# Kernel tuning notes

Measured on AMD Instinct MI355X. Metric: run time of the kernel, lower is better.

## Reference

```python
import jax, jax.numpy as jnp
import numpy as np

C_A = 768; C_S = 384; C_Z = 128; H = 16; D = C_A // H
B = 1; N = 4096; NQ = 32; NK = 128; NB = N // NQ
EPS = 1e-5


def _ln(x):
    # layernorm without learned affine (affine applied by caller where present)
    m = jnp.mean(x, axis=-1, keepdims=True)
    v = jnp.mean((x - m) ** 2, axis=-1, keepdims=True)
    return (x - m) * jax.lax.rsqrt(v + EPS)


def setup_inputs() -> dict:
    key = jax.random.key(0)
    ks = jax.random.split(key, 16)
    w = lambda k, shp: jax.random.normal(k, shp, dtype=jnp.float32) * 0.02
    return dict(
        a=jax.random.normal(ks[0], (B, N, C_A), jnp.float32),
        s=jax.random.normal(ks[1], (B, N, C_S), jnp.float32),
        z=jax.random.normal(ks[2], (B, NB, NQ, NK, C_Z), jnp.float32),
        adaln_gamma_s=jnp.ones((C_S,), jnp.float32),
        adaln_ws=w(ks[3], (C_S, C_A)),
        adaln_bs=jnp.zeros((C_A,), jnp.float32),
        adaln_wskip=w(ks[4], (C_S, C_A)),
        lnz_gamma=jnp.ones((C_Z,), jnp.float32),
        wz=w(ks[5], (C_Z, H)),
        wq=w(ks[6], (C_A, C_A)), bq=jnp.zeros((C_A,), jnp.float32),
        wk=w(ks[7], (C_A, C_A)),
        wv=w(ks[8], (C_A, C_A)),
        wg=w(ks[9], (C_A, C_A)), bg=jnp.ones((C_A,), jnp.float32),
        wo=w(ks[10], (C_A, C_A)), bo=jnp.zeros((C_A,), jnp.float32),
        w_last=w(ks[11], (C_S, C_A)),
        b_last=jnp.full((C_A,), -2.0, jnp.float32),  # biasinit = -2.0
        n_queries=NQ, n_keys=NK,
    )


def _forward(a, s, z, adaln_gamma_s, adaln_ws, adaln_bs, adaln_wskip,
             lnz_gamma, wz, wq, bq, wk, wv, wg, bg, wo, bo,
             w_last, b_last, n_queries, n_keys):
    Bq, Nq, _ = a.shape
    nb = Nq // n_queries
    # AdaptiveLayerNorm (AF3 Alg 26): a <- sigmoid(Lin(s_ln)) * LN(a) + LinNoBias(s_ln)
    s_ln = _ln(s) * adaln_gamma_s
    a_ln = jax.nn.sigmoid(s_ln @ adaln_ws + adaln_bs) * _ln(a) + s_ln @ adaln_wskip
    # pair bias: LN(z) (no offset) -> per-head bias, permuted to [B,H,nb,nq,nk]
    bias = (_ln(z) * lnz_gamma) @ wz                    # [B, nb, nq, nk, H]
    bias = jnp.transpose(bias, (0, 4, 1, 2, 3))          # [B, H, nb, nq, nk]
    # projections (q has bias; k/v no bias)
    q = (a_ln @ wq + bq).reshape(Bq, nb, n_queries, H, D)
    k = (a_ln @ wk).reshape(Bq, Nq, H, D)
    v = (a_ln @ wv).reshape(Bq, Nq, H, D)
    # local window: query block w covers [w*nq, (w+1)*nq); keys are nk centered on it
    start = jnp.arange(nb) * n_queries + n_queries // 2 - n_keys // 2
    kidx = start[:, None] + jnp.arange(n_keys)[None, :]  # [nb, nk]
    valid = (kidx >= 0) & (kidx < Nq)
    kidx = jnp.clip(kidx, 0, Nq - 1)
    k_loc = k[:, kidx]                                    # [B, nb, nk, H, D]
    v_loc = v[:, kidx]
    scale = 1.0 / float(np.sqrt(D))
    scores = jnp.einsum('bwqhd,bwkhd->bhwqk', q, k_loc) * scale + bias
    scores = jnp.where(valid[None, None, :, None, :], scores, -1e9)
    p = jax.nn.softmax(scores, axis=-1)
    o = jnp.einsum('bhwqk,bwkhd->bwqhd', p, v_loc).reshape(Bq, Nq, C_A)
    # gating, output projection, final sigmoid gate from raw s
    o = (jax.nn.sigmoid(a_ln @ wg + bg) * o) @ wo + bo
    return jax.nn.sigmoid(s @ w_last + b_last) * o


def reference(a, s, z, adaln_gamma_s, adaln_ws, adaln_bs, adaln_wskip,
              lnz_gamma, wz, wq, bq, wk, wv, wg, bg, wo, bo,
              w_last, b_last, n_queries, n_keys):
    return _forward(a, s, z, adaln_gamma_s, adaln_ws, adaln_bs, adaln_wskip,
                    lnz_gamma, wz, wq, bq, wk, wv, wg, bg, wo, bo,
                    w_last, b_last, n_queries, n_keys)
```

## Files before the change

kernel.cpp:

```cpp
#include <hip/hip_runtime.h>
#include <hip/hip_bf16.h>
#include <math.h>

#define N_TOK 4096
#define CA 768
#define CS 384
#define CZ 128
#define NHEAD 16
#define DH 48
#define NQW 32
#define NKW 128
#define NBLK 128

typedef __attribute__((ext_vector_type(8))) short short8;
typedef __attribute__((ext_vector_type(4))) float float4v;
typedef __attribute__((ext_vector_type(4))) unsigned short ushort4v;

__device__ __forceinline__ float sigmoidf_(float x){ return 1.0f/(1.0f+__expf(-x)); }

__device__ __forceinline__ unsigned short f2bf(float x){
  unsigned u = __float_as_uint(x);
  unsigned r = (u + 0x7FFFu + ((u>>16)&1u)) >> 16;
  return (unsigned short)r;
}
__device__ __forceinline__ float bf2f(unsigned short b){
  return __uint_as_float(((unsigned)b)<<16);
}
__device__ __forceinline__ short8 cvt8(const float* xv){
  union { short8 v; unsigned short u[8]; } H;
  #pragma unroll
  for (int j=0;j<8;j++) H.u[j] = f2bf(xv[j]);
  return H.v;
}
__device__ __forceinline__ short8 cvt8pk(const float* x){
  union { short8 v; unsigned u32[4]; } H;
  #pragma unroll
  for (int i=0;i<4;i++)
    asm("v_cvt_pk_bf16_f32 %0, %1, %2" : "=v"(H.u32[i]) : "v"(x[2*i]), "v"(x[2*i+1]));
  return H.v;
}

__device__ __forceinline__ void gload_lds16(const void* gsrc, void* ldst){
  __builtin_amdgcn_global_load_lds(
    (const __attribute__((address_space(1))) void*)gsrc,
    (__attribute__((address_space(3))) void*)ldst, 16, 0, 0);
}

__device__ __forceinline__ int xcd_swz(int wg, int nwg){
  int cpx = nwg >> 3;
  return (wg & 7)*cpx + (wg >> 3);
}

__global__ __launch_bounds__(256) void prep_zbias_kernel(
  const float* __restrict__ z, const float* __restrict__ lnz_gamma,
  const float* __restrict__ wz, unsigned short* __restrict__ bias3,
  const float* __restrict__ s, const float* __restrict__ adaln_gamma,
  unsigned short* __restrict__ s_ln_h, unsigned short* __restrict__ s_h,
  const float* __restrict__ a, float* __restrict__ a_n,
  const float* __restrict__ ws, const float* __restrict__ wskip,
  const float* __restrict__ wq, const float* __restrict__ wk,
  const float* __restrict__ wv, const float* __restrict__ wg,
  const float* __restrict__ wo, const float* __restrict__ wlast,
  unsigned short* __restrict__ Wt1, unsigned short* __restrict__ Wt2,
  unsigned short* __restrict__ Wt3, unsigned short* __restrict__ Wt4,
  const float* __restrict__ bq, const float* __restrict__ bg,
  float* __restrict__ biasq)
{
  union PZ {
    float tile[64][65];
    float zbuf[2][2][2048];
  };
  __shared__ PZ sm;
  int bid = blockIdx.x;
  int tid = threadIdx.x;

  if (bid < 2048){
    int wave = tid>>6, lane = tid&63;
    if (wave >= 2) return;
    int lr = lane&15, quad = lane>>4;

    short8 bwh[4];
    float w1 = 0.f;
    #pragma unroll
    for (int ks=0;ks<4;ks++){
      float wv_[8];
      #pragma unroll
      for (int j=0;j<8;j++){
        int k = ks*32 + quad*8 + j;
        wv_[j] = wz[k*NHEAD + lr]*lnz_gamma[k];
        w1 += wv_[j];
      }
      bwh[ks] = cvt8pk(wv_);
    }
    w1 += __shfl_xor(w1, 16);
    w1 += __shfl_xor(w1, 32);

    size_t group = (size_t)bid*2 + wave;
    const float* zg = z + group*(size_t)(NKW*CZ);
    unsigned short* outg = bias3 + group*2048;

    int rsub = lane>>5;
    int csw  = lane&31;
    auto stage = [&](int buf, int b){
      #pragma unroll
      for (int i=0;i<8;i++){
        int r  = 2*i + rsub;
        int gc = csw ^ (r & 7);
        gload_lds16(zg + (size_t)(b*16 + r)*CZ + gc*4, &sm.zbuf[wave][buf][i*256]);
      }
    };

    stage(0, 0);
    int buf = 0;
    #pragma unroll 1
    for (int b=0; b<8; ++b){
      if (b < 7){
        stage(buf^1, b+1);
        asm volatile("s_waitcnt vmcnt(8)" ::: "memory");
      } else {
        asm volatile("s_waitcnt vmcnt(0)" ::: "memory");
      }
      __builtin_amdgcn_sched_barrier(0);

      const float* rowp = &sm.zbuf[wave][buf][lr*128];
      int sswz = lr & 7;
      float4 p[8];
      #pragma unroll
      for (int ks=0;ks<4;ks++){
        int c0 = ks*8 + quad*2;
        p[ks*2]   = *(const float4*)(rowp + (size_t)((c0  )^sswz)*4);
        p[ks*2+1] = *(const float4*)(rowp + (size_t)((c0+1)^sswz)*4);
      }
      float sum=0.f, sq=0.f;
      #pragma unroll
      for (int t=0;t<8;t++){
        sum += p[t].x + p[t].y + p[t].z + p[t].w;
        sq  += p[t].x*p[t].x + p[t].y*p[t].y + p[t].z*p[t].z + p[t].w*p[t].w;
      }
      sum += __shfl_xor(sum,16); sum += __shfl_xor(sum,32);
      sq  += __shfl_xor(sq,16);  sq  += __shfl_xor(sq,32);
      float mean = sum*(1.f/CZ);
      float var  = sq*(1.f/CZ) - mean*mean;
      float rs = rsqrtf(var + 1e-5f);

      float4v c = (float4v){0.f,0.f,0.f,0.f};
      #pragma unroll
      for (int ks=0;ks<4;ks++){
        float xv[8];
        xv[0]=p[ks*2].x;   xv[1]=p[ks*2].y;   xv[2]=p[ks*2].z;   xv[3]=p[ks*2].w;
        xv[4]=p[ks*2+1].x; xv[5]=p[ks*2+1].y; xv[6]=p[ks*2+1].z; xv[7]=p[ks*2+1].w;
        c = __builtin_amdgcn_mfma_f32_16x16x32_bf16(cvt8pk(xv), bwh[ks], c, 0,0,0);
      }

      ushort4v o4;
      #pragma unroll
      for (int r=0;r<4;r++){
        int rrow = quad*4 + r;
        float m_r  = __shfl(mean, rrow);
        float rs_r = __shfl(rs, rrow);
        o4[r] = f2bf(rs_r*(c[r] - m_r*w1));
      }
      *(ushort4v*)(outg + lr*128 + b*16 + quad*4) = o4;
      buf ^= 1;
    }
    return;
  }
  bid -= 2048;

  if (bid < 1024){
    int wave = tid>>6, lane = tid&63;
    int row = bid*4 + wave;
    const float* x = s + (size_t)row*CS;
    float v[6]; float sum=0.f, sq=0.f;
    #pragma unroll
    for (int i=0;i<6;i++){ v[i]=x[lane+64*i]; sum+=v[i]; sq+=v[i]*v[i]; }
    #pragma unroll
    for (int off=32; off; off>>=1){ sum+=__shfl_xor(sum,off); sq+=__shfl_xor(sq,off); }
    float m = sum*(1.f/CS);
    float var = sq*(1.f/CS)-m*m;
    float rs = rsqrtf(var+1e-5f);
    #pragma unroll
    for (int i=0;i<6;i++){
      int c = lane+64*i;
      s_ln_h[(size_t)row*CS+c] = f2bf((v[i]-m)*rs*adaln_gamma[c]);
      s_h[(size_t)row*CS+c]    = f2bf(v[i]);
    }
    return;
  }
  bid -= 1024;

  if (bid < 1024){
    int wave = tid>>6, lane = tid&63;
    int row = bid*4 + wave;
    const float* x = a + (size_t)row*CA;
    float v[12]; float sum=0.f, sq=0.f;
    #pragma unroll
    for (int i=0;i<12;i++){ v[i]=x[lane+64*i]; sum+=v[i]; sq+=v[i]*v[i]; }
    #pragma unroll
    for (int off=32; off; off>>=1){ sum+=__shfl_xor(sum,off); sq+=__shfl_xor(sq,off); }
    float m = sum*(1.f/CA);
    float var = sq*(1.f/CA)-m*m;
    float rs = rsqrtf(var+1e-5f);
    float* o = a_n + (size_t)row*CA;
    #pragma unroll
    for (int i=0;i<12;i++) o[lane+64*i] = (v[i]-m)*rs;
    return;
  }
  bid -= 1024;

  if (bid < 936){
    const float* src; unsigned short* dst; int K; int local;
    if      (bid < 72)  { src=ws;    dst=Wt1;                   K=CS; local=bid; }
    else if (bid < 144) { src=wskip; dst=Wt1 + (size_t)768*CS;  K=CS; local=bid-72; }
    else if (bid < 288) { src=wq;    dst=Wt2;                   K=CA; local=bid-144; }
    else if (bid < 432) { src=wk;    dst=Wt2 + (size_t)768*CA;  K=CA; local=bid-288; }
    else if (bid < 576) { src=wv;    dst=Wt2 + (size_t)1536*CA; K=CA; local=bid-432; }
    else if (bid < 720) { src=wg;    dst=Wt2 + (size_t)2304*CA; K=CA; local=bid-576; }
    else if (bid < 864) { src=wo;    dst=Wt3;                   K=CA; local=bid-720; }
    else                { src=wlast; dst=Wt4;                   K=CS; local=bid-864; }
    int ktiles = K/64;
    int kb = (local % ktiles)*64, nb = (local / ktiles)*64;
    int c = tid & 63, r0 = tid >> 6;
    #pragma unroll
    for (int i=0;i<16;i++){
      int r = r0 + 4*i;
      sm.tile[r][c] = src[(size_t)(kb+r)*CA + nb + c];
    }
    __syncthreads();
    #pragma unroll
    for (int i=0;i<16;i++){
      int r = r0 + 4*i;
      dst[(size_t)(nb+r)*K + kb + c] = f2bf(sm.tile[c][r]);
    }
    return;
  }
  bid -= 936;

  int i = bid*256 + tid;
  float v = 0.f;
  if (i < 768) v = bq[i];
  else if (i >= 2304) v = bg[i-2304];
  biasq[i] = v;
}

__global__ __launch_bounds__(256) void adaln_gemm(
  const unsigned short* __restrict__ A, const unsigned short* __restrict__ Bt,
  const float* __restrict__ bs, const float* __restrict__ a_n,
  unsigned short* __restrict__ outh)
{
  __shared__ unsigned short Ash[64*32];
  __shared__ unsigned short B1sh[128*32];
  __shared__ unsigned short B2sh[128*32];

  int tid = threadIdx.x;
  int w = tid >> 6, lane = tid & 63;
  int lr = lane & 15, quad = lane >> 4;
  int wg = xcd_swz(blockIdx.y*gridDim.x + blockIdx.x, gridDim.x*gridDim.y);
  int bx = wg % gridDim.x, by = wg / gridDim.x;
  int m0 = by*64, n0 = bx*128;
  int mbase = (w&1)*32, nbase = (w>>1)*64;

  float4v acc1[2][4], acc2[2][4];
  #pragma unroll
  for (int i=0;i<2;i++)
    #pragma unroll
    for (int j=0;j<4;j++){
      acc1[i][j] = (float4v){0.f,0.f,0.f,0.f};
      acc2[i][j] = (float4v){0.f,0.f,0.f,0.f};
    }

  int growB = w*32 + (lane>>2);
  int growA = w*16 + (lane>>2);
  int gcol8 = (lane&3)*8;

  for (int k0=0; k0<CS; k0+=32){
    __syncthreads();
    gload_lds16(A + (size_t)(m0 + growA)*CS + k0 + gcol8, &Ash[(w*16)*32]);
    #pragma unroll
    for (int i=0;i<2;i++){
      int rB = growB + i*16;
      gload_lds16(Bt + (size_t)(n0 + rB)*CS + k0 + gcol8, &B1sh[(w*32 + i*16)*32]);
      gload_lds16(Bt + (size_t)(768 + n0 + rB)*CS + k0 + gcol8, &B2sh[(w*32 + i*16)*32]);
    }
    __syncthreads();

    short8 af[2], b1f[4], b2f[4];
    #pragma unroll
    for (int mi=0;mi<2;mi++)
      af[mi] = *(const short8*)&Ash[(mbase + mi*16 + lr)*32 + quad*8];
    #pragma unroll
    for (int ni=0;ni<4;ni++){
      b1f[ni] = *(const short8*)&B1sh[(nbase + ni*16 + lr)*32 + quad*8];
      b2f[ni] = *(const short8*)&B2sh[(nbase + ni*16 + lr)*32 + quad*8];
    }
    #pragma unroll
    for (int mi=0;mi<2;mi++)
      #pragma unroll
      for (int ni=0;ni<4;ni++){
        acc1[mi][ni] = __builtin_amdgcn_mfma_f32_16x16x32_bf16(af[mi], b1f[ni], acc1[mi][ni], 0,0,0);
        acc2[mi][ni] = __builtin_amdgcn_mfma_f32_16x16x32_bf16(af[mi], b2f[ni], acc2[mi][ni], 0,0,0);
      }
  }

  #pragma unroll
  for (int ni=0;ni<4;ni++){
    int col = n0 + nbase + ni*16 + lr;
    float bsv = bs[col];
    #pragma unroll
    for (int mi=0;mi<2;mi++){
      #pragma unroll
      for (int reg=0;reg<4;reg++){
        int row = m0 + mbase + mi*16 + quad*4 + reg;
        float v = sigmoidf_(acc1[mi][ni][reg] + bsv)*a_n[(size_t)row*CA + col] + acc2[mi][ni][reg];
        outh[(size_t)row*CA + col] = f2bf(v);
      }
    }
  }
}

__global__ __launch_bounds__(256) void final_gemm(
  const unsigned short* __restrict__ A1, const unsigned short* __restrict__ B1,
  const float* __restrict__ bias1,
  const unsigned short* __restrict__ A2, const unsigned short* __restrict__ B2,
  const float* __restrict__ bias2,
  float* __restrict__ outp)
{
  __shared__ unsigned short Ash[64*32];
  __shared__ unsigned short Bsh[128*32];

  int tid = threadIdx.x;
  int w = tid >> 6, lane = tid & 63;
  int lr = lane & 15, quad = lane >> 4;
  int wg = xcd_swz(blockIdx.y*gridDim.x + blockIdx.x, gridDim.x*gridDim.y);
  int bx = wg % gridDim.x, by = wg / gridDim.x;
  int m0 = by*64, n0 = bx*128;
  int mbase = (w&1)*32, nbase = (w>>1)*64;

  float4v acc1[2][4], acc2[2][4];
  #pragma unroll
  for (int i=0;i<2;i++)
    #pragma unroll
    for (int j=0;j<4;j++){
      acc1[i][j] = (float4v){0.f,0.f,0.f,0.f};
      acc2[i][j] = (float4v){0.f,0.f,0.f,0.f};
    }

  int growB = w*32 + (lane>>2);
  int growA = w*16 + (lane>>2);
  int gcol8 = (lane&3)*8;

  const int NT1 = CA/32, NT2 = CS/32, NT = NT1+NT2;
  #pragma unroll 1
  for (int t=0; t<NT; ++t){
    const unsigned short* Ap; const unsigned short* Bp; int K, k0;
    if (t < NT1){ Ap=A1; Bp=B1; K=CA; k0=t*32; }
    else        { Ap=A2; Bp=B2; K=CS; k0=(t-NT1)*32; }
    __syncthreads();
    gload_lds16(Ap + (size_t)(m0 + growA)*K + k0 + gcol8, &Ash[(w*16)*32]);
    #pragma unroll
    for (int i=0;i<2;i++){
      int rB = growB + i*16;
      gload_lds16(Bp + (size_t)(n0 + rB)*K + k0 + gcol8, &Bsh[(w*32 + i*16)*32]);
    }
    __syncthreads();

    short8 af[2], bf[4];
    #pragma unroll
    for (int mi=0;mi<2;mi++)
      af[mi] = *(const short8*)&Ash[(mbase + mi*16 + lr)*32 + quad*8];
    #pragma unroll
    for (int ni=0;ni<4;ni++)
      bf[ni] = *(const short8*)&Bsh[(nbase + ni*16 + lr)*32 + quad*8];
    if (t < NT1){
      #pragma unroll
      for (int mi=0;mi<2;mi++)
        #pragma unroll
        for (int ni=0;ni<4;ni++)
          acc1[mi][ni] = __builtin_amdgcn_mfma_f32_16x16x32_bf16(af[mi], bf[ni], acc1[mi][ni], 0,0,0);
    } else {
      #pragma unroll
      for (int mi=0;mi<2;mi++)
        #pragma unroll
        for (int ni=0;ni<4;ni++)
          acc2[mi][ni] = __builtin_amdgcn_mfma_f32_16x16x32_bf16(af[mi], bf[ni], acc2[mi][ni], 0,0,0);
    }
  }

  #pragma unroll
  for (int ni=0;ni<4;ni++){
    int col = n0 + nbase + ni*16 + lr;
    float bv1 = bias1[col];
    float bv2 = bias2[col];
    #pragma unroll
    for (int mi=0;mi<2;mi++){
      #pragma unroll
      for (int reg=0;reg<4;reg++){
        int row = m0 + mbase + mi*16 + quad*4 + reg;
        outp[(size_t)row*CA + col] = sigmoidf_(acc2[mi][ni][reg] + bv2)*(acc1[mi][ni][reg] + bv1);
      }
    }
  }
}

__global__ __launch_bounds__(256) void qkvg_gemm(
  const unsigned short* __restrict__ A1, const unsigned short* __restrict__ B1,
  const float* __restrict__ bias1, unsigned short* __restrict__ outp)
{
  __shared__ unsigned short Ash[128*32];
  __shared__ unsigned short Bsh[128*32];

  int tid = threadIdx.x;
  int w = tid >> 6, lane = tid & 63;
  int lr = lane & 15, quad = lane >> 4;
  int wg = xcd_swz(blockIdx.y*gridDim.x + blockIdx.x, gridDim.x*gridDim.y);
  int bx = wg % gridDim.x, by = wg / gridDim.x;
  int m0 = by*128, n0 = bx*128;
  int mbase = (w&1)*64, nbase = (w>>1)*64;

  float4v acc1[4][4];
  #pragma unroll
  for (int i=0;i<4;i++)
    #pragma unroll
    for (int j=0;j<4;j++)
      acc1[i][j] = (float4v){0.f,0.f,0.f,0.f};

  int grow = w*32 + (lane>>2);
  int gcol8 = (lane&3)*8;

  for (int k0=0; k0<CA; k0+=32){
    __syncthreads();
    #pragma unroll
    for (int i=0;i<2;i++){
      int rA = grow + i*16;
      gload_lds16(A1 + (size_t)(m0 + rA)*CA + k0 + gcol8, &Ash[(w*32 + i*16)*32]);
      gload_lds16(B1 + (size_t)(n0 + rA)*CA + k0 + gcol8, &Bsh[(w*32 + i*16)*32]);
    }
    __syncthreads();

    short8 af[4], bf[4];
    #pragma unroll
    for (int mi=0;mi<4;mi++)
      af[mi] = *(const short8*)&Ash[(mbase + mi*16 + lr)*32 + quad*8];
    #pragma unroll
    for (int ni=0;ni<4;ni++)
      bf[ni] = *(const short8*)&Bsh[(nbase + ni*16 + lr)*32 + quad*8];
    #pragma unroll
    for (int mi=0;mi<4;mi++)
      #pragma unroll
      for (int ni=0;ni<4;ni++)
        acc1[mi][ni] = __builtin_amdgcn_mfma_f32_16x16x32_bf16(af[mi], bf[ni], acc1[mi][ni], 0,0,0);
  }

  #pragma unroll
  for (int ni=0;ni<4;ni++){
    int col = n0 + nbase + ni*16 + lr;
    float bv = bias1[col];
    #pragma unroll
    for (int mi=0;mi<4;mi++){
      #pragma unroll
      for (int reg=0;reg<4;reg++){
        int row = m0 + mbase + mi*16 + quad*4 + reg;
        outp[(size_t)row*3072 + col] = f2bf(acc1[mi][ni][reg] + bv);
      }
    }
  }
}

__global__ __launch_bounds__(256) void attn_kernel(
  const unsigned short* __restrict__ qh,
  const unsigned short* __restrict__ bias3h,
  unsigned short* __restrict__ og)
{
  __shared__ unsigned short Vs[128*192];
  __shared__ unsigned short Pb[4][32*40];
  int tid = threadIdx.x, wave = tid>>6, lane = tid&63;
  int lr = lane&15, quad = lane>>4;
  int w = blockIdx.x, h = blockIdx.y*4 + wave;
  int start = w*NQW - 48;
  const float scale = 0.14433756729740643f;

  {
    int hbase = blockIdx.y*4*DH;
    #pragma unroll
    for (int it=0; it<12; ++it){
      int c = it*256 + tid;
      int key = c/24, cc = c - key*24;
      int kr = min(max(start+key,0),N_TOK-1);
      short8 v = *(const short8*)&qh[(size_t)kr*3072 + 1536 + hbase + cc*8];
      int cs = cc ^ (((key>>3)&3)*2);
      *(short8*)&Vs[key*192 + cs*8] = v;
    }
  }

  short8 zero8 = {0,0,0,0,0,0,0,0};

  short8 aq[2][2];
  #pragma unroll
  for (int mt=0;mt<2;mt++){
    int row = w*NQW + mt*16 + lr;
    const unsigned short* qp = qh + (size_t)row*3072 + h*DH;
    aq[mt][0] = *(const short8*)(qp + quad*8);
    aq[mt][1] = (quad<2) ? *(const short8*)(qp + 32 + quad*8) : zero8;
  }

  float4v c[2][8];
  #pragma unroll
  for (int mt=0;mt<2;mt++)
    #pragma unroll
    for (int nt=0;nt<8;nt++) c[mt][nt] = (float4v){0.f,0.f,0.f,0.f};

  #pragma unroll 2
  for (int nt=0;nt<8;nt++){
    int krc = min(max(start + nt*16 + lr,0),N_TOK-1);
    const unsigned short* kp = qh + (size_t)krc*3072 + 768 + h*DH;
    short8 bk0 = *(const short8*)(kp + quad*8);
    short8 bk1 = (quad<2) ? *(const short8*)(kp + 32 + quad*8) : zero8;
    #pragma unroll
    for (int mt=0;mt<2;mt++){
      c[mt][nt] = __builtin_amdgcn_mfma_f32_16x16x32_bf16(aq[mt][0], bk0, c[mt][nt], 0,0,0);
      c[mt][nt] = __builtin_amdgcn_mfma_f32_16x16x32_bf16(aq[mt][1], bk1, c[mt][nt], 0,0,0);
    }
  }

  float rmax[2][4], rsum[2][4];
  #pragma unroll
  for (int mt=0;mt<2;mt++)
    #pragma unroll
    for (int r=0;r<4;r++){ rmax[mt][r] = -3.0e38f; rsum[mt][r] = 0.f; }

  #pragma unroll
  for (int nt=0;nt<8;nt++){
    int key = start + nt*16 + lr;
    bool valid = (key>=0) && (key<N_TOK);
    #pragma unroll
    for (int mt=0;mt<2;mt++){
      #pragma unroll
      for (int r=0;r<4;r++){
        int q = mt*16 + quad*4 + r;
        float bv = bf2f(bias3h[(((size_t)(w*NQW+q))*NHEAD + h)*128 + nt*16 + lr]);
        float v = valid ? (c[mt][nt][r]*scale + bv) : -1e9f;
        c[mt][nt][r] = v;
        rmax[mt][r] = fmaxf(rmax[mt][r], v);
      }
    }
  }
  #pragma unroll
  for (int mt=0;mt<2;mt++)
    #pragma unroll
    for (int r=0;r<4;r++){
      float m = rmax[mt][r];
      m = fmaxf(m, __shfl_xor(m,1)); m = fmaxf(m, __shfl_xor(m,2));
      m = fmaxf(m, __shfl_xor(m,4)); m = fmaxf(m, __shfl_xor(m,8));
      rmax[mt][r] = m;
    }
  #pragma unroll
  for (int nt=0;nt<8;nt++)
    #pragma unroll
    for (int mt=0;mt<2;mt++)
      #pragma unroll
      for (int r=0;r<4;r++){
        float e = __expf(c[mt][nt][r] - rmax[mt][r]);
        c[mt][nt][r] = e;
        rsum[mt][r] += e;
      }
  #pragma unroll
  for (int mt=0;mt<2;mt++)
    #pragma unroll
    for (int r=0;r<4;r++){
      float sv = rsum[mt][r];
      sv += __shfl_xor(sv,1); sv += __shfl_xor(sv,2);
      sv += __shfl_xor(sv,4); sv += __shfl_xor(sv,8);
      rsum[mt][r] = 1.f/sv;
    }

  __syncthreads();

  unsigned short* ph = &Pb[wave][0];
  float4v o[2][3];
  #pragma unroll
  for (int mt=0;mt<2;mt++)
    #pragma unroll
    for (int no=0;no<3;no++) o[mt][no] = (float4v){0.f,0.f,0.f,0.f};

  #pragma unroll 1
  for (int c2=0;c2<2;c2++){
    #pragma unroll 1
    for (int ks=0;ks<2;ks++){
      int ntb = c2*4 + ks*2;
      #pragma unroll
      for (int t=0;t<2;t++){
        int nt = ntb + t;
        #pragma unroll
        for (int mt=0;mt<2;mt++){
          #pragma unroll
          for (int r=0;r<4;r++){
            int q = mt*16 + quad*4 + r;
            ph[q*40 + t*16 + lr] = f2bf(c[mt][nt][r]*rsum[mt][r]);
          }
        }
      }
      short8 pa[2];
      #pragma unroll
      for (int mt=0;mt<2;mt++)
        pa[mt] = *(const short8*)&ph[(mt*16+lr)*40 + quad*8];
      #pragma unroll
      for (int no=0;no<3;no++){
        union { short8 v; unsigned short u[8]; } V;
        int col = wave*DH + no*16 + lr;
        int chunk = col >> 3;
        int cs = (chunk ^ (quad*2))*8 + (col & 7);
        #pragma unroll
        for (int j=0;j<8;j++){
          int key = c2*64 + ks*32 + quad*8 + j;
          V.u[j] = Vs[key*192 + cs];
        }
        #pragma unroll
        for (int mt=0;mt<2;mt++)
          o[mt][no] = __builtin_amdgcn_mfma_f32_16x16x32_bf16(pa[mt], V.v, o[mt][no], 0,0,0);
      }
    }
  }

  #pragma unroll
  for (int mt=0;mt<2;mt++){
    #pragma unroll
    for (int no=0;no<3;no++){
      int d = no*16 + lr;
      #pragma unroll
      for (int r=0;r<4;r++){
        int q = mt*16 + quad*4 + r;
        size_t grow = (size_t)(w*NQW + q);
        float g = bf2f(qh[grow*3072 + 2304 + h*DH + d]);
        og[grow*CA + h*DH + d] = f2bf(o[mt][no][r] * sigmoidf_(g));
      }
    }
  }
}

extern "C" void kernel_launch(void* const* d_in, const int* in_sizes, int n_in,
                              void* d_out, int out_size, void* d_ws, size_t ws_size,
                              hipStream_t stream)
{
  const float* a            = (const float*)d_in[0];
  const float* s            = (const float*)d_in[1];
  const float* z            = (const float*)d_in[2];
  const float* adaln_gamma  = (const float*)d_in[3];
  const float* adaln_ws     = (const float*)d_in[4];
  const float* adaln_bs     = (const float*)d_in[5];
  const float* adaln_wskip  = (const float*)d_in[6];
  const float* lnz_gamma    = (const float*)d_in[7];
  const float* wz           = (const float*)d_in[8];
  const float* wq           = (const float*)d_in[9];
  const float* bq           = (const float*)d_in[10];
  const float* wk           = (const float*)d_in[11];
  const float* wv           = (const float*)d_in[12];
  const float* wg           = (const float*)d_in[13];
  const float* bg           = (const float*)d_in[14];
  const float* wo           = (const float*)d_in[15];
  const float* bo           = (const float*)d_in[16];
  const float* w_last       = (const float*)d_in[17];
  const float* b_last       = (const float*)d_in[18];
  float* out = (float*)d_out;

  char* base = (char*)d_ws;
  size_t off = 0;
  auto alloc = [&](size_t bytes)->char*{ char* p = base + off; off += (bytes + 255) & ~(size_t)255; return p; };

  unsigned short* s_ln_h = (unsigned short*)alloc((size_t)N_TOK*CS*2);
  unsigned short* s_h    = (unsigned short*)alloc((size_t)N_TOK*CS*2);
  float*          a_n    = (float*)alloc((size_t)N_TOK*CA*4);
  unsigned short* a_ln_h = (unsigned short*)alloc((size_t)N_TOK*CA*2);
  unsigned short* og_h   = (unsigned short*)alloc((size_t)N_TOK*CA*2);
  unsigned short* Wt1    = (unsigned short*)alloc((size_t)1536*CS*2);
  unsigned short* Wt2    = (unsigned short*)alloc((size_t)3072*CA*2);
  unsigned short* Wt3    = (unsigned short*)alloc((size_t)CA*CA*2);
  unsigned short* Wt4    = (unsigned short*)alloc((size_t)CA*CS*2);
  unsigned short* bias3h = (unsigned short*)alloc((size_t)N_TOK*NHEAD*NKW*2);
  unsigned short* qkvg_h = (unsigned short*)alloc((size_t)N_TOK*3072*2);
  float*          biasq  = (float*)alloc((size_t)3072*4);

  prep_zbias_kernel<<<dim3(2048+1024+1024+936+12), 256, 0, stream>>>(
      z, lnz_gamma, wz, bias3h,
      s, adaln_gamma, s_ln_h, s_h, a, a_n,
      adaln_ws, adaln_wskip, wq, wk, wv, wg, wo, w_last,
      Wt1, Wt2, Wt3, Wt4, bq, bg, biasq);

  adaln_gemm<<<dim3(CA/128, N_TOK/64), 256, 0, stream>>>(s_ln_h, Wt1, adaln_bs, a_n, a_ln_h);

  qkvg_gemm<<<dim3(3072/128, N_TOK/128), 256, 0, stream>>>(a_ln_h, Wt2, biasq, qkvg_h);

  attn_kernel<<<dim3(NBLK, 4), 256, 0, stream>>>(qkvg_h, bias3h, og_h);

  final_gemm<<<dim3(CA/128, N_TOK/64), 256, 0, stream>>>(
      og_h, Wt3, bo, s_h, Wt4, b_last, out);
}
```

Before: 221.0 us.

## Double GEMM K-tile to 64 with XOR-swizzled LDS layout

The three MFMA GEMM kernels (adaln, final, qkvg) now stage 64-wide K slices instead of 32, which halves the number of barrier pairs per K loop. The LDS tile is stored with an XOR swizzle on 16-byte chunks, applied both when loading from global and when reading fragments, so the fragment reads avoid bank conflicts. This doubles shared memory per block, which may reduce occupancy, especially in the adaln kernel with its two B tiles.

```diff
diff --git a/kernel.cpp b/kernel.cpp
--- a/kernel.cpp
+++ b/kernel.cpp
@@ -248,9 +248,9 @@
   const float* __restrict__ bs, const float* __restrict__ a_n,
   unsigned short* __restrict__ outh)
 {
-  __shared__ unsigned short Ash[64*32];
-  __shared__ unsigned short B1sh[128*32];
-  __shared__ unsigned short B2sh[128*32];
+  __shared__ unsigned short Ash[64*64];
+  __shared__ unsigned short B1sh[128*64];
+  __shared__ unsigned short B2sh[128*64];
 
   int tid = threadIdx.x;
   int w = tid >> 6, lane = tid & 63;
@@ -269,37 +269,45 @@
       acc2[i][j] = (float4v){0.f,0.f,0.f,0.f};
     }
 
-  int growB = w*32 + (lane>>2);
-  int growA = w*16 + (lane>>2);
-  int gcol8 = (lane&3)*8;
-
-  for (int k0=0; k0<CS; k0+=32){
+  int rsub = lane>>3;
+  int gcs  = ((lane&7) ^ rsub)*8;
+  int rkey = lr & 7;
+
+  for (int k0=0; k0<CS; k0+=64){
     __syncthreads();
-    gload_lds16(A + (size_t)(m0 + growA)*CS + k0 + gcol8, &Ash[(w*16)*32]);
-    #pragma unroll
-    for (int i=0;i<2;i++){
-      int rB = growB + i*16;
-      gload_lds16(Bt + (size_t)(n0 + rB)*CS + k0 + gcol8, &B1sh[(w*32 + i*16)*32]);
-      gload_lds16(Bt + (size_t)(768 + n0 + rB)*CS + k0 + gcol8, &B2sh[(w*32 + i*16)*32]);
+    #pragma unroll
+    for (int it=0; it<2; ++it){
+      int r = it*32 + w*8 + rsub;
+      gload_lds16(A + (size_t)(m0 + r)*CS + k0 + gcs, &Ash[(it*32 + w*8)*64]);
+    }
+    #pragma unroll
+    for (int it=0; it<4; ++it){
+      int r = it*32 + w*8 + rsub;
+      gload_lds16(Bt + (size_t)(n0 + r)*CS + k0 + gcs, &B1sh[(it*32 + w*8)*64]);
+      gload_lds16(Bt + (size_t)(768 + n0 + r)*CS + k0 + gcs, &B2sh[(it*32 + w*8)*64]);
     }
     __syncthreads();
 
-    short8 af[2], b1f[4], b2f[4];
-    #pragma unroll
-    for (int mi=0;mi<2;mi++)
-      af[mi] = *(const short8*)&Ash[(mbase + mi*16 + lr)*32 + quad*8];
-    #pragma unroll
-    for (int ni=0;ni<4;ni++){
-      b1f[ni] = *(const short8*)&B1sh[(nbase + ni*16 + lr)*32 + quad*8];
-      b2f[ni] = *(const short8*)&B2sh[(nbase + ni*16 + lr)*32 + quad*8];
-    }
-    #pragma unroll
-    for (int mi=0;mi<2;mi++)
+    #pragma unroll
+    for (int ks=0; ks<2; ++ks){
+      int slot = ((ks*4 + quad) ^ rkey)*8;
+      short8 af[2], b1f[4], b2f[4];
+      #pragma unroll
+      for (int mi=0;mi<2;mi++)
+        af[mi] = *(const short8*)&Ash[(mbase + mi*16 + lr)*64 + slot];
       #pragma unroll
       for (int ni=0;ni<4;ni++){
-        acc1[mi][ni] = __builtin_amdgcn_mfma_f32_16x16x32_bf16(af[mi], b1f[ni], acc1[mi][ni], 0,0,0);
-        acc2[mi][ni] = __builtin_amdgcn_mfma_f32_16x16x32_bf16(af[mi], b2f[ni], acc2[mi][ni], 0,0,0);
-      }
+        b1f[ni] = *(const short8*)&B1sh[(nbase + ni*16 + lr)*64 + slot];
+        b2f[ni] = *(const short8*)&B2sh[(nbase + ni*16 + lr)*64 + slot];
+      }
+      #pragma unroll
+      for (int mi=0;mi<2;mi++)
+        #pragma unroll
+        for (int ni=0;ni<4;ni++){
+          acc1[mi][ni] = __builtin_amdgcn_mfma_f32_16x16x32_bf16(af[mi], b1f[ni], acc1[mi][ni], 0,0,0);
+          acc2[mi][ni] = __builtin_amdgcn_mfma_f32_16x16x32_bf16(af[mi], b2f[ni], acc2[mi][ni], 0,0,0);
+        }
+    }
   }
 
   #pragma unroll
@@ -325,8 +333,8 @@
   const float* __restrict__ bias2,
   float* __restrict__ outp)
 {
-  __shared__ unsigned short Ash[64*32];
-  __shared__ unsigned short Bsh[128*32];
+  __shared__ unsigned short Ash[64*64];
+  __shared__ unsigned short Bsh[128*64];
 
   int tid = threadIdx.x;
   int w = tid >> 6, lane = tid & 63;
@@ -345,44 +353,52 @@
       acc2[i][j] = (float4v){0.f,0.f,0.f,0.f};
     }
 
-  int growB = w*32 + (lane>>2);
-  int growA = w*16 + (lane>>2);
-  int gcol8 = (lane&3)*8;
-
-  const int NT1 = CA/32, NT2 = CS/32, NT = NT1+NT2;
+  int rsub = lane>>3;
+  int gcs  = ((lane&7) ^ rsub)*8;
+  int rkey = lr & 7;
+
+  const int NT1 = CA/64, NT2 = CS/64, NT = NT1+NT2;
   #pragma unroll 1
   for (int t=0; t<NT; ++t){
     const unsigned short* Ap; const unsigned short* Bp; int K, k0;
-    if (t < NT1){ Ap=A1; Bp=B1; K=CA; k0=t*32; }
-    else        { Ap=A2; Bp=B2; K=CS; k0=(t-NT1)*32; }
+    if (t < NT1){ Ap=A1; Bp=B1; K=CA; k0=t*64; }
+    else        { Ap=A2; Bp=B2; K=CS; k0=(t-NT1)*64; }
     __syncthreads();
-    gload_lds16(Ap + (size_t)(m0 + growA)*K + k0 + gcol8, &Ash[(w*16)*32]);
-    #pragma unroll
-    for (int i=0;i<2;i++){
-      int rB = growB + i*16;
-      gload_lds16(Bp + (size_t)(n0 + rB)*K + k0 + gcol8, &Bsh[(w*32 + i*16)*32]);
+    #pragma unroll
+    for (int it=0; it<2; ++it){
+      int r = it*32 + w*8 + rsub;
+      gload_lds16(Ap + (size_t)(m0 + r)*K + k0 + gcs, &Ash[(it*32 + w*8)*64]);
+    }
+    #pragma unroll
+    for (int it=0; it<4; ++it){
+      int r = it*32 + w*8 + rsub;
+      gload_lds16(Bp + (size_t)(n0 + r)*K + k0 + gcs, &Bsh[(it*32 + w*8)*64]);
     }
     __syncthreads();
 
-    short8 af[2], bf[4];
-    #pragma unroll
-    for (int mi=0;mi<2;mi++)
-      af[mi] = *(const short8*)&Ash[(mbase + mi*16 + lr)*32 + quad*8];
-    #pragma unroll
-    for (int ni=0;ni<4;ni++)
-      bf[ni] = *(const short8*)&Bsh[(nbase + ni*16 + lr)*32 + quad*8];
-    if (t < NT1){
+    #pragma unroll
+    for (int ks=0; ks<2; ++ks){
+      int slot = ((ks*4 + quad) ^ rkey)*8;
+      short8 af[2], bf[4];
       #pragma unroll
       for (int mi=0;mi<2;mi++)
+        af[mi] = *(const short8*)&Ash[(mbase + mi*16 + lr)*64 + slot];
+      #pragma unroll
+      for (int ni=0;ni<4;ni++)
+        bf[ni] = *(const short8*)&Bsh[(nbase + ni*16 + lr)*64 + slot];
+      if (t < NT1){
         #pragma unroll
-        for (int ni=0;ni<4;ni++)
-          acc1[mi][ni] = __builtin_amdgcn_mfma_f32_16x16x32_bf16(af[mi], bf[ni], acc1[mi][ni], 0,0,0);
-    } else {
-      #pragma unroll
-      for (int mi=0;mi<2;mi++)
+        for (int mi=0;mi<2;mi++)
+          #pragma unroll
+          for (int ni=0;ni<4;ni++)
+            acc1[mi][ni] = __builtin_amdgcn_mfma_f32_16x16x32_bf16(af[mi], bf[ni], acc1[mi][ni], 0,0,0);
+      } else {
         #pragma unroll
-        for (int ni=0;ni<4;ni++)
-          acc2[mi][ni] = __builtin_amdgcn_mfma_f32_16x16x32_bf16(af[mi], bf[ni], acc2[mi][ni], 0,0,0);
+        for (int mi=0;mi<2;mi++)
+          #pragma unroll
+          for (int ni=0;ni<4;ni++)
+            acc2[mi][ni] = __builtin_amdgcn_mfma_f32_16x16x32_bf16(af[mi], bf[ni], acc2[mi][ni], 0,0,0);
+      }
     }
   }
 
@@ -406,8 +422,8 @@
   const unsigned short* __restrict__ A1, const unsigned short* __restrict__ B1,
   const float* __restrict__ bias1, unsigned short* __restrict__ outp)
 {
-  __shared__ unsigned short Ash[128*32];
-  __shared__ unsigned short Bsh[128*32];
+  __shared__ unsigned short Ash[128*64];
+  __shared__ unsigned short Bsh[128*64];
 
   int tid = threadIdx.x;
   int w = tid >> 6, lane = tid & 63;
@@ -424,31 +440,36 @@
     for (int j=0;j<4;j++)
       acc1[i][j] = (float4v){0.f,0.f,0.f,0.f};
 
-  int grow = w*32 + (lane>>2);
-  int gcol8 = (lane&3)*8;
-
-  for (int k0=0; k0<CA; k0+=32){
+  int rsub = lane>>3;
+  int gcs  = ((lane&7) ^ rsub)*8;
+  int rkey = lr & 7;
+
+  for (int k0=0; k0<CA; k0+=64){
     __syncthreads();
     #pragma unroll
-    for (int i=0;i<2;i++){
-      int rA = grow + i*16;
-      gload_lds16(A1 + (size_t)(m0 + rA)*CA + k0 + gcol8, &Ash[(w*32 + i*16)*32]);
-      gload_lds16(B1 + (size_t)(n0 + rA)*CA + k0 + gcol8, &Bsh[(w*32 + i*16)*32]);
+    for (int it=0; it<4; ++it){
+      int r = it*32 + w*8 + rsub;
+      gload_lds16(A1 + (size_t)(m0 + r)*CA + k0 + gcs, &Ash[(it*32 + w*8)*64]);
+      gload_lds16(B1 + (size_t)(n0 + r)*CA + k0 + gcs, &Bsh[(it*32 + w*8)*64]);
     }
     __syncthreads();
 
-    short8 af[4], bf[4];
-    #pragma unroll
-    for (int mi=0;mi<4;mi++)
-      af[mi] = *(const short8*)&Ash[(mbase + mi*16 + lr)*32 + quad*8];
-    #pragma unroll
-    for (int ni=0;ni<4;ni++)
-      bf[ni] = *(const short8*)&Bsh[(nbase + ni*16 + lr)*32 + quad*8];
-    #pragma unroll
-    for (int mi=0;mi<4;mi++)
+    #pragma unroll
+    for (int ks=0; ks<2; ++ks){
+      int slot = ((ks*4 + quad) ^ rkey)*8;
+      short8 af[4], bf[4];
+      #pragma unroll
+      for (int mi=0;mi<4;mi++)
+        af[mi] = *(const short8*)&Ash[(mbase + mi*16 + lr)*64 + slot];
       #pragma unroll
       for (int ni=0;ni<4;ni++)
-        acc1[mi][ni] = __builtin_amdgcn_mfma_f32_16x16x32_bf16(af[mi], bf[ni], acc1[mi][ni], 0,0,0);
+        bf[ni] = *(const short8*)&Bsh[(nbase + ni*16 + lr)*64 + slot];
+      #pragma unroll
+      for (int mi=0;mi<4;mi++)
+        #pragma unroll
+        for (int ni=0;ni<4;ni++)
+          acc1[mi][ni] = __builtin_amdgcn_mfma_f32_16x16x32_bf16(af[mi], bf[ni], acc1[mi][ni], 0,0,0);
+    }
   }
 
   #pragma unroll
```

New measurement: 217.5 us. No clear change (-1.6%).
